# Kernel tuning notes

Measured on AMD Instinct MI355X. Metric: run time of the kernel, lower is better.

## Reference

```python
import jax, jax.numpy as jnp
import numpy as np
from jax.scipy.linalg import expm

N = 512      # state dim
TMAX = 1024  # integration steps
STEP = 0.01  # step size
G = 1.0      # slope restriction (Sigma diag bounded by 1/G)
EPS = 1e-05
BS = 128


def setup_inputs() -> dict:
    key = jax.random.key(0)
    ks = jax.random.split(key, 6)
    return {
        "X0": jax.random.normal(ks[0], (BS, N), jnp.float32),
        "A_raw": jax.random.normal(ks[1], (1, 1), jnp.float32),
        "Theta_raw": jnp.ones((N, N), jnp.float32),
        "U_raw": jax.random.normal(ks[2], (N, N), jnp.float32),
        "Sigma_raw": jax.random.normal(ks[3], (N, N), jnp.float32),
        "V_raw": jax.random.normal(ks[4], (N, N), jnp.float32),
        "bx_raw": jax.random.normal(ks[5], (N, 1), jnp.float32) * 0.01,
    }


def _skew(Z):
    T = jnp.triu(Z, 1)
    return T - T.T


def reference(X0, A_raw, Theta_raw, U_raw, Sigma_raw, V_raw, bx_raw):
    # --- parametrizations ---
    a = jnp.abs(A_raw)[0, 0] + EPS                      # Positive: A = -a*I
    theta_d = jnp.abs(jnp.diagonal(Theta_raw)) + EPS    # Pos_Diag: Theta = diag(theta_d)
    U = expm(_skew(U_raw))                              # orthogonal
    V = expm(_skew(V_raw))                              # orthogonal
    sigma_d = (1.0 / G) * jnp.exp(-jnp.diagonal(Sigma_raw) ** 2)  # Bounded_PositiveDiag

    # B = Theta^{-1} @ U @ Sigma @ V^T @ Theta  (diag matmuls as row/col scalings)
    B = (U * sigma_d[None, :]) @ V.T                    # U @ Sigma @ V^T
    B = (B * theta_d[None, :]) / theta_d[:, None]       # Theta^{-1} @ (.) @ Theta

    Xi0 = X0.T                                          # (n, bs)
    bx = bx_raw                                         # (n, 1), broadcasts over batch

    def body(Xi, _):
        Xn = Xi + STEP * (-a * Xi + B @ jax.nn.relu(Xi) + bx)
        return Xn, Xn

    _, rest = jax.lax.scan(body, Xi0, None, length=TMAX - 1)  # (tmax-1, n, bs)
    X = jnp.concatenate([Xi0[None], rest], axis=0)            # (tmax, n, bs)
    return jnp.transpose(X, (2, 0, 1))                        # (bs, tmax, n)
```

## Files before the change

### kernel.cpp

```cpp
#include <hip/hip_runtime.h>
#include <cstddef>

#define NN 512
#define BSZ 128
#define TMAXN 1024
#define STEP_F 0.01f
#define EPS_F 1e-05f
#define MATSZ (NN*NN)
#define MAT2 (2*MATSZ)
#define OUT_TN (TMAXN*NN)
#define SKEW_SCALE 0.03125f
#define NBLOCKS 64
#define NDOM 16
#define DCOLS 8

typedef __bf16 bf16x8 __attribute__((ext_vector_type(8)));
typedef float f32x4 __attribute__((ext_vector_type(4)));
typedef unsigned short u16x4 __attribute__((ext_vector_type(4)));
typedef unsigned u32x4 __attribute__((ext_vector_type(4)));
typedef unsigned long long ull;


__global__ void prep_params(const float* __restrict__ A_raw,
                            const float* __restrict__ Theta_raw,
                            const float* __restrict__ Sigma_raw,
                            const float* __restrict__ bx_raw,
                            float* __restrict__ params,
                            float* __restrict__ theta,
                            float* __restrict__ sigma,
                            float* __restrict__ bx)
{
    int i = threadIdx.x;
    if (i == 0) params[0] = fabsf(A_raw[0]) + EPS_F;
    theta[i] = fabsf(Theta_raw[i*NN + i]) + EPS_F;
    float sd = Sigma_raw[i*NN + i];
    sigma[i] = expf(-sd*sd);
    bx[i] = bx_raw[i];
}

__global__ void build_S(const float* __restrict__ U_raw,
                        const float* __restrict__ V_raw,
                        float* __restrict__ S)
{
    int idx = blockIdx.x * 256 + threadIdx.x;
    int z = idx >> 18;
    int rem = idx & (MATSZ - 1);
    int i = rem >> 9;
    int j = rem & (NN - 1);
    const float* src = (z == 0) ? U_raw : V_raw;
    float v = 0.0f;
    if (i < j)      v = src[i*NN + j];
    else if (i > j) v = -src[j*NN + i];
    S[idx] = v * SKEW_SCALE;
}

__global__ __launch_bounds__(256) void mm64(const float* __restrict__ A,
                                            const float* __restrict__ Bm,
                                            float* __restrict__ C,
                                            int accflag)
{
    int z = blockIdx.z;
    A  += (size_t)z * MATSZ;
    Bm += (size_t)z * MATSZ;
    C  += (size_t)z * MATSZ;

    __shared__ float As[16][68];
    __shared__ float Bs[16][68];

    int tid = threadIdx.x;
    int tx = tid & 15;
    int ty = tid >> 4;
    int row0 = blockIdx.y * 64;
    int col0 = blockIdx.x * 64;

    float acc[4][4] = {{0.f}};

    for (int k0 = 0; k0 < NN; k0 += 16) {
        {
            int i = tid >> 2;
            int j = (tid & 3) << 2;
            float4 av = *reinterpret_cast<const float4*>(&A[(size_t)(row0 + i)*NN + k0 + j]);
            As[j+0][i] = av.x; As[j+1][i] = av.y; As[j+2][i] = av.z; As[j+3][i] = av.w;
        }
        {
            int bi = tid >> 4;
            int bj = (tid & 15) << 2;
            float4 bv = *reinterpret_cast<const float4*>(&Bm[(size_t)(k0 + bi)*NN + col0 + bj]);
            *reinterpret_cast<float4*>(&Bs[bi][bj]) = bv;
        }
        __syncthreads();
#pragma unroll
        for (int k = 0; k < 16; ++k) {
            float a0 = As[k][ty], a1 = As[k][ty+16], a2 = As[k][ty+32], a3 = As[k][ty+48];
            float b0 = Bs[k][tx], b1 = Bs[k][tx+16], b2 = Bs[k][tx+32], b3 = Bs[k][tx+48];
            acc[0][0] += a0*b0; acc[0][1] += a0*b1; acc[0][2] += a0*b2; acc[0][3] += a0*b3;
            acc[1][0] += a1*b0; acc[1][1] += a1*b1; acc[1][2] += a1*b2; acc[1][3] += a1*b3;
            acc[2][0] += a2*b0; acc[2][1] += a2*b1; acc[2][2] += a2*b2; acc[2][3] += a2*b3;
            acc[3][0] += a3*b0; acc[3][1] += a3*b1; acc[3][2] += a3*b2; acc[3][3] += a3*b3;
        }
        __syncthreads();
    }

#pragma unroll
    for (int mi = 0; mi < 4; ++mi) {
        size_t r = (size_t)(row0 + ty + 16*mi);
#pragma unroll
        for (int mj = 0; mj < 4; ++mj) {
            size_t cidx = r*NN + col0 + tx + 16*mj;
            float v = acc[mi][mj];
            if (accflag) v += C[cidx];
            C[cidx] = v;
        }
    }
}

__global__ void combo3(const float* __restrict__ S, const float* __restrict__ S2,
                       const float* __restrict__ S3, const float* __restrict__ S4,
                       float* __restrict__ Q0, float* __restrict__ Q1,
                       float* __restrict__ Q2)
{
    const float C0 = 1.0f, C1 = 1.0f, C2 = 0.5f, C3 = 1.0f/6.0f;
    const float C4 = 1.0f/24.0f, C5 = 1.0f/120.0f, C6 = 1.0f/720.0f, C7 = 1.0f/5040.0f;
    const float C8 = 1.0f/40320.0f, C9 = 1.0f/362880.0f, C10 = 1.0f/3628800.0f;
    const float C11 = 1.0f/39916800.0f, C12 = 1.0f/479001600.0f;
    int idx = blockIdx.x * 256 + threadIdx.x;
    int rem = idx & (MATSZ - 1);
    int i = rem >> 9;
    int j = rem & (NN - 1);
    float d = (i == j) ? 1.0f : 0.0f;
    float s = S[idx], s2 = S2[idx], s3 = S3[idx], s4 = S4[idx];
    Q0[idx] = C0*d + C1*s + C2*s2 + C3*s3;
    Q1[idx] = C4*d + C5*s + C6*s2 + C7*s3;
    Q2[idx] = C8*d + C9*s + C10*s2 + C11*s3 + C12*s4;
}

__global__ void scale_transpose(const float* __restrict__ EU,
                                const float* __restrict__ EV,
                                const float* __restrict__ sigma,
                                float* __restrict__ Asc,
                                float* __restrict__ VT)
{
    int idx = blockIdx.x * 256 + threadIdx.x;
    int i = idx >> 9;
    int j = idx & (NN - 1);
    Asc[idx] = EU[idx] * sigma[j];
    VT[idx]  = EV[j*NN + i];
}

__global__ void finalize_Bsplit(const float* __restrict__ Bmm,
                                const float* __restrict__ theta,
                                __bf16* __restrict__ Bh,
                                __bf16* __restrict__ Bl)
{
    int idx = blockIdx.x * 256 + threadIdx.x;
    int r = idx >> 9;
    int k = idx & (NN - 1);
    float v = Bmm[idx] * theta[k] / theta[r];
    __bf16 h = (__bf16)v;
    Bh[idx] = h;
    Bl[idx] = (__bf16)(v - (float)h);
}

__global__ void init_x(const float* __restrict__ X0,
                       float* __restrict__ xb0,
                       float* __restrict__ out)
{
    int idx = blockIdx.x * 256 + threadIdx.x;
    int b = idx >> 9;
    int n = idx & (NN - 1);
    float v = X0[idx];
    xb0[idx] = v;
    out[(size_t)b * OUT_TN + n] = v;
}

__global__ __launch_bounds__(512, 2) void step_persist(
    const float* __restrict__ x0g,
    const __bf16* __restrict__ Bh,
    const __bf16* __restrict__ Bl,
    const float* __restrict__ params,
    const float* __restrict__ bx,
    float* __restrict__ out,
    ull* __restrict__ pay,
    unsigned* __restrict__ flg)
{
    __shared__ char xs[65536];
    __shared__ unsigned pubstage[1024];
    int tid = threadIdx.x;
    int bid = blockIdx.x;
    int dom = bid >> 2;
    int rg  = bid & 3;
    int w = tid >> 6;
    int l = tid & 63;

    int r0 = rg*128 + w*16;
    int arow = l & 15;
    int kch  = l >> 4;
    f32x4 ah[16], al[16];
    {
        const __bf16* bhrow = Bh + (size_t)(r0 + arow)*NN + kch*8;
        const __bf16* blrow = Bl + (size_t)(r0 + arow)*NN + kch*8;
#pragma unroll
        for (int ks = 0; ks < 16; ++ks) {
            ah[ks] = *reinterpret_cast<const f32x4*>(bhrow + ks*32);
            al[ks] = *reinterpret_cast<const f32x4*>(blrow + ks*32);
        }
    }
#pragma unroll
    for (int ks = 0; ks < 16; ++ks) {
        asm volatile("" : "+v"(ah[ks]));
        asm volatile("" : "+v"(al[ks]));
    }

    int c_l  = l & 15;
    int real = (c_l < DCOLS);
    int crow = r0 + (l >> 4)*4;
    int crow_loc = w*16 + (l >> 4)*4;
    int ccol = dom*DCOLS + (c_l & 7);
    float c0 = 1.0f - STEP_F * (params[0]);
    float4 bv = *reinterpret_cast<const float4*>(&bx[crow]);
    int xsw   = (c_l & 7) << 4;
    int xfrag = c_l * 1024;
    int own_ad = xfrag + ((2*crow) ^ xsw);

    int sc = tid >> 5;
    int ks_l = tid & 31;
    int scb = sc * 1024;
    int ssw = (sc & 7) << 4;

    {
        const float* src = x0g + (size_t)(dom*DCOLS + (sc & 7))*NN;
#pragma unroll
        for (int i = 0; i < 16; ++i) {
            int k = i*32 + ks_l;
            float x = (sc < 8) ? fmaxf(src[k], 0.0f) : 0.0f;
            __bf16 hh = (__bf16)x;
            __bf16 ll = (__bf16)(x - (float)hh);
            int ad = scb + ((2*k) ^ ssw);
            *reinterpret_cast<__bf16*>(&xs[ad]) = hh;
            *reinterpret_cast<__bf16*>(&xs[16384 + ad]) = ll;
            if (sc >= 8) {
                *reinterpret_cast<__bf16*>(&xs[32768 + ad]) = hh;
                *reinterpret_cast<__bf16*>(&xs[49152 + ad]) = ll;
            }
        }
    }
    float4 xo = *reinterpret_cast<const float4*>(&x0g[(size_t)ccol*NN + crow]);

    for (int t = 1; t < TMAXN; ++t) {
        __syncthreads();

        int curoff = ((t-1) & 1) * 32768;
        int nxtoff = (t & 1) * 32768;

        f32x4 acc0 = {0,0,0,0}, acc1 = {0,0,0,0}, acc2 = {0,0,0,0};
#pragma unroll
        for (int ks = 0; ks < 16; ++ks) {
            int ad = curoff + xfrag + (((ks*32 + kch*8) * 2) ^ xsw);
            bf16x8 xh = __builtin_bit_cast(bf16x8, *reinterpret_cast<const f32x4*>(&xs[ad]));
            bf16x8 xl = __builtin_bit_cast(bf16x8, *reinterpret_cast<const f32x4*>(&xs[16384 + ad]));
            acc0 = __builtin_amdgcn_mfma_f32_16x16x32_bf16(__builtin_bit_cast(bf16x8, ah[ks]), xh, acc0, 0, 0, 0);
            acc1 = __builtin_amdgcn_mfma_f32_16x16x32_bf16(__builtin_bit_cast(bf16x8, al[ks]), xh, acc1, 0, 0, 0);
            acc2 = __builtin_amdgcn_mfma_f32_16x16x32_bf16(__builtin_bit_cast(bf16x8, ah[ks]), xl, acc2, 0, 0, 0);
        }

        float4 nv;
        nv.x = c0*xo.x + STEP_F*(acc0[0] + acc1[0] + acc2[0] + bv.x);
        nv.y = c0*xo.y + STEP_F*(acc0[1] + acc1[1] + acc2[1] + bv.y);
        nv.z = c0*xo.z + STEP_F*(acc0[2] + acc1[2] + acc2[2] + bv.z);
        nv.w = c0*xo.w + STEP_F*(acc0[3] + acc1[3] + acc2[3] + bv.w);
        xo = nv;

        if (t < TMAXN - 1) {
            float v4[4] = {nv.x, nv.y, nv.z, nv.w};
            u16x4 hv, lv;
            u32x4 pk;
#pragma unroll
            for (int j = 0; j < 4; ++j) {
                float x = fmaxf(v4[j], 0.0f);
                __bf16 hh = (__bf16)x;
                __bf16 ll = (__bf16)(x - (float)hh);
                unsigned short hb = __builtin_bit_cast(unsigned short, hh);
                unsigned short lb = __builtin_bit_cast(unsigned short, ll);
                hv[j] = hb; lv[j] = lb;
                pk[j] = (unsigned)hb | ((unsigned)lb << 16);
            }
            if (real) {
                *reinterpret_cast<u16x4*>(&xs[nxtoff + own_ad]) = hv;
                *reinterpret_cast<u16x4*>(&xs[16384 + nxtoff + own_ad]) = lv;
                *reinterpret_cast<u32x4*>(&pubstage[c_l*128 + crow_loc]) = pk;
            }

            __syncthreads();

            int par = t & 1;
            ull pv_own = reinterpret_cast<ull*>(pubstage)[tid];
            size_t pubBase = ((size_t)(par*NDOM + dom)*4 + rg) * 512;
            __hip_atomic_store(&pay[pubBase + tid], pv_own,
                               __ATOMIC_RELAXED, __HIP_MEMORY_SCOPE_AGENT);

            __syncthreads();
            unsigned* fline = flg + (size_t)(par*NDOM + dom) * 16;
            if (tid == 0) {
                __hip_atomic_store(&fline[rg], (unsigned)t,
                                   __ATOMIC_RELAXED, __HIP_MEMORY_SCOPE_AGENT);
            }
            if (real) {
                *reinterpret_cast<float4*>(&out[(size_t)ccol*OUT_TN + (size_t)t*NN + crow]) = nv;
            }

            unsigned tu = (unsigned)t;
            for (;;) {
                ull f01 = __hip_atomic_load((ull*)fline,     __ATOMIC_RELAXED, __HIP_MEMORY_SCOPE_AGENT);
                ull f23 = __hip_atomic_load((ull*)fline + 1, __ATOMIC_RELAXED, __HIP_MEMORY_SCOPE_AGENT);
                unsigned f0 = (unsigned)f01, f1 = (unsigned)(f01 >> 32);
                unsigned f2 = (unsigned)f23, f3 = (unsigned)(f23 >> 32);
                bool ok = (rg == 0 || f0 >= tu) && (rg == 1 || f1 >= tu)
                       && (rg == 2 || f2 >= tu) && (rg == 3 || f3 >= tu);
                if (ok) break;
                __builtin_amdgcn_s_sleep(1);
            }
            asm volatile("" ::: "memory");
            __builtin_amdgcn_sched_barrier(0);

            ull pv[3];
            int rgs[3];
#pragma unroll
            for (int rr = 0; rr < 3; ++rr) {
                rgs[rr] = (rg + 1 + rr) & 3;
                size_t b = ((size_t)(par*NDOM + dom)*4 + rgs[rr]) * 512;
                pv[rr] = __hip_atomic_load(&pay[b + tid],
                             __ATOMIC_RELAXED, __HIP_MEMORY_SCOPE_AGENT);
            }

            int ucol = tid >> 6;
            int urow = (tid & 63) * 2;
            int usw = (ucol & 7) << 4;
            int ubase = nxtoff + ucol*1024;
#pragma unroll
            for (int rr = 0; rr < 3; ++rr) {
                int row = rgs[rr]*128 + urow;
                unsigned a = (unsigned)pv[rr];
                unsigned b2 = (unsigned)(pv[rr] >> 32);
                int ad0 = ubase + ((2*row) ^ usw);
                int ad1 = ubase + ((2*(row+1)) ^ usw);
                *reinterpret_cast<unsigned short*>(&xs[ad0]) = (unsigned short)a;
                *reinterpret_cast<unsigned short*>(&xs[16384 + ad0]) = (unsigned short)(a >> 16);
                *reinterpret_cast<unsigned short*>(&xs[ad1]) = (unsigned short)b2;
                *reinterpret_cast<unsigned short*>(&xs[16384 + ad1]) = (unsigned short)(b2 >> 16);
            }
        } else {
            if (real) {
                *reinterpret_cast<float4*>(&out[(size_t)ccol*OUT_TN + (size_t)t*NN + crow]) = nv;
            }
        }
    }
}


extern "C" void kernel_launch(void* const* d_in, const int* in_sizes, int n_in,
                              void* d_out, int out_size, void* d_ws, size_t ws_size,
                              hipStream_t stream)
{
    const float* X0        = (const float*)d_in[0];
    const float* A_raw     = (const float*)d_in[1];
    const float* Theta_raw = (const float*)d_in[2];
    const float* U_raw     = (const float*)d_in[3];
    const float* Sigma_raw = (const float*)d_in[4];
    const float* V_raw     = (const float*)d_in[5];
    const float* bx_raw    = (const float*)d_in[6];
    float* out = (float*)d_out;

    float* S   = out;
    float* S2  = out + 1*MAT2;
    float* S3  = out + 2*MAT2;
    float* S4  = out + 3*MAT2;
    float* Q2b = out + 4*MAT2;
    float* Q1b = out + 5*MAT2;
    float* Q0b = out + 6*MAT2;

    char* wsc = (char*)d_ws;
    __bf16* Bh = (__bf16*)wsc;
    __bf16* Bl = (__bf16*)(wsc + 524288);
    float* xb0 = (float*)(wsc + 1048576);
    float* params = (float*)(wsc + 1048576 + 262144);
    float* theta  = params + 64;
    float* sigma  = theta + 512;
    float* bx     = sigma + 512;
    ull* pay      = (ull*)(wsc + 1572864);
    unsigned* flg = (unsigned*)(wsc + 1572864 + 524288);

    prep_params<<<1, 512, 0, stream>>>(A_raw, Theta_raw, Sigma_raw, bx_raw,
                                       params, theta, sigma, bx);
    build_S<<<MAT2/256, 256, 0, stream>>>(U_raw, V_raw, S);

    mm64<<<dim3(8,8,2), 256, 0, stream>>>(S,  S,   S2,  0);
    mm64<<<dim3(8,8,2), 256, 0, stream>>>(S2, S,   S3,  0);
    mm64<<<dim3(8,8,2), 256, 0, stream>>>(S2, S2,  S4,  0);
    combo3<<<MAT2/256, 256, 0, stream>>>(S, S2, S3, S4, Q0b, Q1b, Q2b);
    mm64<<<dim3(8,8,2), 256, 0, stream>>>(S4, Q2b, Q1b, 1);
    mm64<<<dim3(8,8,2), 256, 0, stream>>>(S4, Q1b, Q0b, 1);
    float* Pa = Q0b; float* Pb = Q2b;
    for (int q = 0; q < 5; ++q) {
        mm64<<<dim3(8,8,2), 256, 0, stream>>>(Pa, Pa, Pb, 0);
        float* t2 = Pa; Pa = Pb; Pb = t2;
    }

    scale_transpose<<<MATSZ/256, 256, 0, stream>>>(Pa, Pa + MATSZ, sigma,
                                                   S, S + MATSZ);
    mm64<<<dim3(8,8,1), 256, 0, stream>>>(S, S + MATSZ, S2, 0);
    finalize_Bsplit<<<MATSZ/256, 256, 0, stream>>>(S2, theta, Bh, Bl);

    init_x<<<BSZ*NN/256, 256, 0, stream>>>(X0, xb0, out);

    hipMemsetAsync(flg, 0, 2048, stream);

    void* args[] = { (void*)&xb0, (void*)&Bh, (void*)&Bl,
                     (void*)&params, (void*)&bx, (void*)&out,
                     (void*)&pay, (void*)&flg };
    hipLaunchCooperativeKernel((const void*)step_persist, dim3(NBLOCKS), dim3(512),
                               args, 0, stream);
}
```

Before: 3.033 ms.

## Replace flag-based cross-block exchange with self-tagged data packets

Each published value is now packed into a 64-bit word that also carries the timestep tag. Consumers poll the data words directly until all tags match, so the separate flag array, the shared-memory staging buffer and two block-wide barriers per step are gone. The aim is a shorter inter-block synchronisation chain on each of the 1023 sequential steps. The cost is twice the payload traffic per exchange and spin loops that poll six words per thread instead of two flag words.

```diff
diff --git a/kernel.cpp b/kernel.cpp
--- a/kernel.cpp
+++ b/kernel.cpp
@@ -17,7 +17,6 @@
 typedef __bf16 bf16x8 __attribute__((ext_vector_type(8)));
 typedef float f32x4 __attribute__((ext_vector_type(4)));
 typedef unsigned short u16x4 __attribute__((ext_vector_type(4)));
-typedef unsigned u32x4 __attribute__((ext_vector_type(4)));
 typedef unsigned long long ull;
 
 
@@ -180,11 +179,9 @@
     const float* __restrict__ params,
     const float* __restrict__ bx,
     float* __restrict__ out,
-    ull* __restrict__ pay,
-    unsigned* __restrict__ flg)
+    ull* __restrict__ pkt)
 {
     __shared__ char xs[65536];
-    __shared__ unsigned pubstage[1024];
     int tid = threadIdx.x;
     int bid = blockIdx.x;
     int dom = bid >> 2;
@@ -246,6 +243,10 @@
     }
     float4 xo = *reinterpret_cast<const float4*>(&x0g[(size_t)ccol*NN + crow]);
 
+    int rgs[3];
+#pragma unroll
+    for (int rr = 0; rr < 3; ++rr) rgs[rr] = (rg + 1 + rr) & 3;
+
     for (int t = 1; t < TMAXN; ++t) {
         __syncthreads();
 
@@ -271,82 +272,66 @@
         xo = nv;
 
         if (t < TMAXN - 1) {
+            int par = t & 1;
             float v4[4] = {nv.x, nv.y, nv.z, nv.w};
             u16x4 hv, lv;
-            u32x4 pk;
 #pragma unroll
             for (int j = 0; j < 4; ++j) {
                 float x = fmaxf(v4[j], 0.0f);
                 __bf16 hh = (__bf16)x;
-                __bf16 ll = (__bf16)(x - (float)hh);
-                unsigned short hb = __builtin_bit_cast(unsigned short, hh);
-                unsigned short lb = __builtin_bit_cast(unsigned short, ll);
-                hv[j] = hb; lv[j] = lb;
-                pk[j] = (unsigned)hb | ((unsigned)lb << 16);
+                hv[j] = __builtin_bit_cast(unsigned short, hh);
+                lv[j] = __builtin_bit_cast(unsigned short, (__bf16)(x - (float)hh));
             }
             if (real) {
+                ull tagb = ((ull)(unsigned)t) << 32;
+                ull* pub = pkt + (((size_t)par*NDOM + dom)*4 + rg)*1024
+                               + (size_t)(c_l*128 + crow_loc);
+#pragma unroll
+                for (int j = 0; j < 4; ++j) {
+                    ull pkv = (ull)hv[j] | ((ull)lv[j] << 16) | tagb;
+                    __hip_atomic_store(&pub[j], pkv, __ATOMIC_RELAXED,
+                                       __HIP_MEMORY_SCOPE_AGENT);
+                }
                 *reinterpret_cast<u16x4*>(&xs[nxtoff + own_ad]) = hv;
                 *reinterpret_cast<u16x4*>(&xs[16384 + nxtoff + own_ad]) = lv;
-                *reinterpret_cast<u32x4*>(&pubstage[c_l*128 + crow_loc]) = pk;
-            }
-
-            __syncthreads();
-
-            int par = t & 1;
-            ull pv_own = reinterpret_cast<ull*>(pubstage)[tid];
-            size_t pubBase = ((size_t)(par*NDOM + dom)*4 + rg) * 512;
-            __hip_atomic_store(&pay[pubBase + tid], pv_own,
-                               __ATOMIC_RELAXED, __HIP_MEMORY_SCOPE_AGENT);
-
-            __syncthreads();
-            unsigned* fline = flg + (size_t)(par*NDOM + dom) * 16;
-            if (tid == 0) {
-                __hip_atomic_store(&fline[rg], (unsigned)t,
-                                   __ATOMIC_RELAXED, __HIP_MEMORY_SCOPE_AGENT);
-            }
-            if (real) {
                 *reinterpret_cast<float4*>(&out[(size_t)ccol*OUT_TN + (size_t)t*NN + crow]) = nv;
             }
 
             unsigned tu = (unsigned)t;
+            ull pv[6];
+            const ull* pb[3];
+#pragma unroll
+            for (int rr = 0; rr < 3; ++rr)
+                pb[rr] = pkt + (((size_t)par*NDOM + dom)*4 + rgs[rr])*1024 + 2*tid;
             for (;;) {
-                ull f01 = __hip_atomic_load((ull*)fline,     __ATOMIC_RELAXED, __HIP_MEMORY_SCOPE_AGENT);
-                ull f23 = __hip_atomic_load((ull*)fline + 1, __ATOMIC_RELAXED, __HIP_MEMORY_SCOPE_AGENT);
-                unsigned f0 = (unsigned)f01, f1 = (unsigned)(f01 >> 32);
-                unsigned f2 = (unsigned)f23, f3 = (unsigned)(f23 >> 32);
-                bool ok = (rg == 0 || f0 >= tu) && (rg == 1 || f1 >= tu)
-                       && (rg == 2 || f2 >= tu) && (rg == 3 || f3 >= tu);
+#pragma unroll
+                for (int rr = 0; rr < 3; ++rr) {
+                    pv[rr*2+0] = __hip_atomic_load(pb[rr],     __ATOMIC_RELAXED, __HIP_MEMORY_SCOPE_AGENT);
+                    pv[rr*2+1] = __hip_atomic_load(pb[rr] + 1, __ATOMIC_RELAXED, __HIP_MEMORY_SCOPE_AGENT);
+                }
+                int ok = 1;
+#pragma unroll
+                for (int q = 0; q < 6; ++q)
+                    ok &= ((unsigned)(pv[q] >> 32) == tu);
                 if (ok) break;
                 __builtin_amdgcn_s_sleep(1);
             }
             asm volatile("" ::: "memory");
             __builtin_amdgcn_sched_barrier(0);
 
-            ull pv[3];
-            int rgs[3];
 #pragma unroll
             for (int rr = 0; rr < 3; ++rr) {
-                rgs[rr] = (rg + 1 + rr) & 3;
-                size_t b = ((size_t)(par*NDOM + dom)*4 + rgs[rr]) * 512;
-                pv[rr] = __hip_atomic_load(&pay[b + tid],
-                             __ATOMIC_RELAXED, __HIP_MEMORY_SCOPE_AGENT);
-            }
-
-            int ucol = tid >> 6;
-            int urow = (tid & 63) * 2;
-            int usw = (ucol & 7) << 4;
-            int ubase = nxtoff + ucol*1024;
-#pragma unroll
-            for (int rr = 0; rr < 3; ++rr) {
-                int row = rgs[rr]*128 + urow;
-                unsigned a = (unsigned)pv[rr];
-                unsigned b2 = (unsigned)(pv[rr] >> 32);
-                int ad0 = ubase + ((2*row) ^ usw);
-                int ad1 = ubase + ((2*(row+1)) ^ usw);
-                *reinterpret_cast<unsigned short*>(&xs[ad0]) = (unsigned short)a;
-                *reinterpret_cast<unsigned short*>(&xs[16384 + ad0]) = (unsigned short)(a >> 16);
-                *reinterpret_cast<unsigned short*>(&xs[ad1]) = (unsigned short)b2;
-                *reinterpret_cast<unsigned short*>(&xs[16384 + ad1]) = (unsigned short)(b2 >> 16);
+#pragma unroll
+                for (int q = 0; q < 2; ++q) {
+                    int vi = 2*tid + q;
+                    int c = vi >> 7;
+                    int row = rgs[rr]*128 + (vi & 127);
+                    ull p = pv[rr*2+q];
+                    int ad = nxtoff + c*1024 + ((2*row) ^ (c << 4));
+                    *reinterpret_cast<unsigned short*>(&xs[ad]) = (unsigned short)p;
+                    *reinterpret_cast<unsigned short*>(&xs[16384 + ad]) =
+                        (unsigned short)(p >> 16);
+                }
             }
         } else {
             if (real) {
@@ -386,8 +371,7 @@
     float* theta  = params + 64;
     float* sigma  = theta + 512;
     float* bx     = sigma + 512;
-    ull* pay      = (ull*)(wsc + 1572864);
-    unsigned* flg = (unsigned*)(wsc + 1572864 + 524288);
+    ull* pkt      = (ull*)(wsc + 1572864);
 
     prep_params<<<1, 512, 0, stream>>>(A_raw, Theta_raw, Sigma_raw, bx_raw,
                                        params, theta, sigma, bx);
@@ -412,11 +396,10 @@
 
     init_x<<<BSZ*NN/256, 256, 0, stream>>>(X0, xb0, out);
 
-    hipMemsetAsync(flg, 0, 2048, stream);
+    hipMemsetAsync(pkt, 0, 2*NDOM*4*1024*8, stream);
 
     void* args[] = { (void*)&xb0, (void*)&Bh, (void*)&Bl,
-                     (void*)&params, (void*)&bx, (void*)&out,
-                     (void*)&pay, (void*)&flg };
+                     (void*)&params, (void*)&bx, (void*)&out, (void*)&pkt };
     hipLaunchCooperativeKernel((const void*)step_persist, dim3(NBLOCKS), dim3(512),
                                args, 0, stream);
 }
```

Result: slower. 3.735 ms (+23.1%).
